# Optimization experiments

Measured on AMD Instinct MI355X. Metric: run time of the kernel, lower is better.

The kernel has to match this reference:

```python
import jax, jax.numpy as jnp
import numpy as np

B, L, HID, NH = 2, 2048, 1024, 16
HD = HID // NH  # 64


def setup_inputs() -> dict:
    key = jax.random.key(0)
    ks = jax.random.split(key, 12)
    s = 1.0 / np.sqrt(HID)
    query = jax.random.normal(ks[0], (B, L, HID), jnp.float32)
    key_t = jax.random.normal(ks[1], (B, L, HID), jnp.float32)
    value = jax.random.normal(ks[2], (B, L, HID), jnp.float32)
    # key padding mask: True = valid token; random lengths in [1024, 2048]
    lengths = jax.random.randint(ks[3], (B,), L // 2, L + 1)
    key_mask = jnp.arange(L)[None, :] < lengths[:, None]  # [B, K] bool
    # attn_mask: True = blocked (causal upper triangle), 2D branch [Q, K]
    attn_mask = jnp.triu(jnp.ones((L, L), jnp.bool_), k=1)
    Wq = jax.random.normal(ks[4], (HID, HID), jnp.float32) * s
    Wk = jax.random.normal(ks[5], (HID, HID), jnp.float32) * s
    Wv = jax.random.normal(ks[6], (HID, HID), jnp.float32) * s
    Wo = jax.random.normal(ks[7], (HID, HID), jnp.float32) * s
    bq = jax.random.normal(ks[8], (HID,), jnp.float32) * 0.01
    bk = jax.random.normal(ks[9], (HID,), jnp.float32) * 0.01
    bv = jax.random.normal(ks[10], (HID,), jnp.float32) * 0.01
    bo = jax.random.normal(ks[11], (HID,), jnp.float32) * 0.01
    return {"query": query, "key": key_t, "value": value,
            "key_mask": key_mask, "attn_mask": attn_mask,
            "Wq": Wq, "bq": bq, "Wk": Wk, "bk": bk,
            "Wv": Wv, "bv": bv, "Wo": Wo, "bo": bo}


def reference(query, key, value, key_mask, attn_mask,
              Wq, bq, Wk, bk, Wv, bv, Wo, bo):
    Bq, Q, _ = query.shape
    K = key.shape[1]
    # projections (torch Linear: x @ W.T + b), split heads -> [B, H, L, HD]
    def proj(x, W, b, L_):
        return (x @ W.T + b).reshape(Bq, L_, NH, HD).transpose(0, 2, 1, 3)
    q = proj(query, Wq, bq, Q)
    k = proj(key, Wk, bk, K)
    v = proj(value, Wv, bv, K)
    scores = jnp.einsum('bhqd,bhkd->bhqk', q, k) / np.sqrt(HD)
    blocked = attn_mask[None, None, :, :]                 # True = blocked
    kmask = key_mask[:, None, None, :]                    # True = valid
    valid = (~blocked) & kmask                            # [B,H,Q,K] (bcast)
    scores = jnp.where(blocked, -10000.0, scores)
    scores = jnp.where(kmask, scores, -10000.0)
    weights = jax.nn.softmax(scores, axis=-1)
    weights = weights * valid.astype(weights.dtype)
    weights = weights / jnp.maximum(weights.sum(-1, keepdims=True), 1e-6)
    attended = jnp.einsum('bhqk,bhkd->bhqd', weights, v)
    attended = attended.transpose(0, 2, 1, 3).reshape(Bq, Q, HID)
    return attended @ Wo.T + bo
```

## Files before the change

### kernel.cpp

```cpp
#include <hip/hip_runtime.h>
#include <hip/hip_bf16.h>
#include <stdint.h>


#define L_SEQ 2048
#define HID 1024
#define NHEAD 16
#define HD 64

typedef __attribute__((ext_vector_type(8))) short bf16x8;
typedef __attribute__((ext_vector_type(8))) unsigned short u16x8;
typedef __attribute__((ext_vector_type(4))) float f32x4;

__device__ __forceinline__ unsigned short f2bf(float f) {
  unsigned int u = __builtin_bit_cast(unsigned int, f);
  u += 0x7fffu + ((u >> 16) & 1u);
  return (unsigned short)(u >> 16);
}

__device__ __forceinline__ unsigned int pk2bf(float a, float b) {
  unsigned int r;
  asm("v_cvt_pk_bf16_f32 %0, %1, %2" : "=v"(r) : "v"(a), "v"(b));
  return r;
}

__device__ __forceinline__ void gl_lds16(const void* g, void* l) {
  __builtin_amdgcn_global_load_lds(
      (const __attribute__((address_space(1))) unsigned int*)(uintptr_t)g,
      (__attribute__((address_space(3))) unsigned int*)(uint32_t)(uintptr_t)l,
      16, 0, 0);
}

__device__ __forceinline__ f32x4 mfma16(bf16x8 a, bf16x8 b, f32x4 c) {
  return __builtin_amdgcn_mfma_f32_16x16x32_bf16(a, b, c, 0, 0, 0);
}

__global__ __launch_bounds__(256)
void convert_all_kernel(const float* __restrict__ q, const float* __restrict__ k,
                        const float* __restrict__ v, const float* __restrict__ wq,
                        const float* __restrict__ wk, const float* __restrict__ wv,
                        const float* __restrict__ wo, const unsigned int* __restrict__ km,
                        unsigned short* __restrict__ qb, unsigned short* __restrict__ kb,
                        unsigned short* __restrict__ vb, unsigned short* __restrict__ wqb,
                        unsigned short* __restrict__ wkb, unsigned short* __restrict__ wvb,
                        unsigned short* __restrict__ wob, int* __restrict__ lens) {
  __shared__ int red[256];
  const int bid = blockIdx.x;
  const int t = threadIdx.x;
  if (bid == 8192) {
    unsigned int w0 = km[0];
    bool u8mode = (w0 != 1u);
    for (int b = 0; b < 2; ++b) {
      int cnt = 0;
      if (u8mode) {
        const unsigned char* p = (const unsigned char*)km + b * L_SEQ;
        for (int i = t; i < L_SEQ; i += 256) cnt += (p[i] != 0) ? 1 : 0;
      } else {
        const unsigned int* p = km + b * L_SEQ;
        for (int i = t; i < L_SEQ; i += 256) cnt += (p[i] != 0) ? 1 : 0;
      }
      red[t] = cnt;
      __syncthreads();
      for (int s = 128; s > 0; s >>= 1) {
        if (t < s) red[t] += red[t + s];
        __syncthreads();
      }
      if (t == 0) lens[b] = red[0];
      __syncthreads();
    }
    return;
  }
  const float* src;
  unsigned short* dst;
  int base;
  if (bid < 6144) {
    int s = bid >> 11;
    base = (bid & 2047) * 2048;
    src = s == 0 ? q : (s == 1 ? k : v);
    dst = s == 0 ? qb : (s == 1 ? kb : vb);
  } else {
    int r = bid - 6144;
    int s = r >> 9;
    base = (r & 511) * 2048;
    src = s == 0 ? wq : (s == 1 ? wk : (s == 2 ? wv : wo));
    dst = s == 0 ? wqb : (s == 1 ? wkb : (s == 2 ? wvb : wob));
  }
  int i = base + t * 8;
  float4 a = *(const float4*)(src + i);
  float4 b4 = *(const float4*)(src + i + 4);
  u16x8 o;
  o[0] = f2bf(a.x); o[1] = f2bf(a.y); o[2] = f2bf(a.z); o[3] = f2bf(a.w);
  o[4] = f2bf(b4.x); o[5] = f2bf(b4.y); o[6] = f2bf(b4.z); o[7] = f2bf(b4.w);
  *(u16x8*)(dst + i) = o;
}

__device__ __forceinline__ void gemm128_bf_core(const unsigned short* __restrict__ A,
                                                const unsigned short* __restrict__ W,
                                                int m0, int n0, int K,
                                                unsigned short* As, unsigned short* Bs,
                                                f32x4 acc[4][4]) {
  const int tid = threadIdx.x;
  const int w = tid >> 6, lane = tid & 63;
  const int l15 = lane & 15, l4 = lane >> 4;
  const int wr = w >> 1, wc = w & 1;
#pragma unroll
  for (int i = 0; i < 4; ++i)
#pragma unroll
    for (int j = 0; j < 4; ++j) acc[i][j] = (f32x4){0.f, 0.f, 0.f, 0.f};

  const int nk = K >> 5;
#pragma unroll
  for (int i = 0; i < 2; ++i) {
    int c = i * 256 + tid;
    int row = c >> 2, col = (c & 3) * 8;
    gl_lds16(A + (size_t)(m0 + row) * K + col, (char*)As + (i * 256 + w * 64) * 16);
    gl_lds16(W + (size_t)(n0 + row) * K + col, (char*)Bs + (i * 256 + w * 64) * 16);
  }
  __syncthreads();

  int cur = 0;
  for (int t = 0; t < nk; ++t) {
    const int k0 = t * 32;
    if (t + 1 < nk) {
#pragma unroll
      for (int i = 0; i < 2; ++i) {
        int c = i * 256 + tid;
        int row = c >> 2, col = (c & 3) * 8;
        gl_lds16(A + (size_t)(m0 + row) * K + k0 + 32 + col,
                 (char*)As + (cur ^ 1) * 8192 + (i * 256 + w * 64) * 16);
        gl_lds16(W + (size_t)(n0 + row) * K + k0 + 32 + col,
                 (char*)Bs + (cur ^ 1) * 8192 + (i * 256 + w * 64) * 16);
      }
    }
    const unsigned short* Asb = As + cur * 4096;
    const unsigned short* Bsb = Bs + cur * 4096;
    bf16x8 af[4], bfr[4];
#pragma unroll
    for (int i = 0; i < 4; ++i)
      af[i] = *(const bf16x8*)(Asb + (wr * 64 + i * 16 + l15) * 32 + l4 * 8);
#pragma unroll
    for (int j = 0; j < 4; ++j)
      bfr[j] = *(const bf16x8*)(Bsb + (wc * 64 + j * 16 + l15) * 32 + l4 * 8);
    __builtin_amdgcn_s_setprio(1);
#pragma unroll
    for (int i = 0; i < 4; ++i)
#pragma unroll
      for (int j = 0; j < 4; ++j) acc[i][j] = mfma16(af[i], bfr[j], acc[i][j]);
    __builtin_amdgcn_s_setprio(0);
    __syncthreads();
    cur ^= 1;
  }
}

__global__ __launch_bounds__(256)
void qkv_gemm_kernel(const unsigned short* __restrict__ qb, const unsigned short* __restrict__ kb,
                     const unsigned short* __restrict__ vb, const unsigned short* __restrict__ wq,
                     const unsigned short* __restrict__ wk, const unsigned short* __restrict__ wv,
                     const float* __restrict__ bq, const float* __restrict__ bk,
                     const float* __restrict__ bv, unsigned short* __restrict__ Qp,
                     unsigned short* __restrict__ Kp, unsigned short* __restrict__ Vtp) {
  __shared__ unsigned short As[2 * 128 * 32];
  __shared__ unsigned short Bs[2 * 128 * 32];
  const int z = blockIdx.z;
  const unsigned short* A = z == 0 ? qb : (z == 1 ? kb : vb);
  const unsigned short* W = z == 0 ? wq : (z == 1 ? wk : wv);
  const float* bias = z == 0 ? bq : (z == 1 ? bk : bv);
  const int m0 = blockIdx.y * 128, n0 = blockIdx.x * 128;
  f32x4 acc[4][4];
  gemm128_bf_core(A, W, m0, n0, HID, As, Bs, acc);

  const int tid = threadIdx.x;
  const int w = tid >> 6, lane = tid & 63;
  const int l15 = lane & 15, l4 = lane >> 4;
  const int wr = w >> 1, wc = w & 1;
  const float scale = (z == 0) ? 0.125f * 1.44269504089f : 1.0f;
  if (z == 2) {
#pragma unroll
    for (int i = 0; i < 4; ++i)
#pragma unroll
      for (int j = 0; j < 4; ++j) {
        int grow0 = m0 + wr * 64 + i * 16 + l4 * 4;
        int gcol = n0 + wc * 64 + j * 16 + l15;
        float bv_ = bias[gcol];
        int bb = grow0 >> 11, ll0 = grow0 & 2047;
        int hh = gcol >> 6, d = gcol & 63;
        uint2 pw;
        pw.x = pk2bf(acc[i][j][0] + bv_, acc[i][j][1] + bv_);
        pw.y = pk2bf(acc[i][j][2] + bv_, acc[i][j][3] + bv_);
        *(uint2*)(&Vtp[((size_t)(bb * NHEAD + hh) * HD + d) * L_SEQ + ll0]) = pw;
      }
  } else {
    unsigned short* P = (z == 0) ? Qp : Kp;
#pragma unroll
    for (int i = 0; i < 4; ++i)
#pragma unroll
      for (int j = 0; j < 4; ++j)
#pragma unroll
        for (int r = 0; r < 4; ++r) {
          int grow = m0 + wr * 64 + i * 16 + l4 * 4 + r;
          int gcol = n0 + wc * 64 + j * 16 + l15;
          float v = (acc[i][j][r] + bias[gcol]) * scale;
          int bb = grow >> 11, ll = grow & 2047;
          int hh = gcol >> 6, d = gcol & 63;
          P[((size_t)(bb * NHEAD + hh) * L_SEQ + ll) * HD + d] = f2bf(v);
        }
  }
}

__global__ __launch_bounds__(256)
void out_gemm_kernel(const unsigned short* __restrict__ att, const unsigned short* __restrict__ wo,
                     const float* __restrict__ bo, float* __restrict__ out) {
  __shared__ unsigned short As[2 * 128 * 32];
  __shared__ unsigned short Bs[2 * 128 * 32];
  const int m0 = blockIdx.y * 128, n0 = blockIdx.x * 128;
  f32x4 acc[4][4];
  gemm128_bf_core(att, wo, m0, n0, HID, As, Bs, acc);

  const int tid = threadIdx.x;
  const int w = tid >> 6, lane = tid & 63;
  const int l15 = lane & 15, l4 = lane >> 4;
  const int wr = w >> 1, wc = w & 1;
#pragma unroll
  for (int i = 0; i < 4; ++i)
#pragma unroll
    for (int j = 0; j < 4; ++j)
#pragma unroll
      for (int r = 0; r < 4; ++r) {
        int grow = m0 + wr * 64 + i * 16 + l4 * 4 + r;
        int gcol = n0 + wc * 64 + j * 16 + l15;
        out[(size_t)grow * HID + gcol] = acc[i][j][r] + bo[gcol];
      }
}

__global__ __launch_bounds__(512)
void attn_kernel(const unsigned short* __restrict__ Qp, const unsigned short* __restrict__ Kp,
                 const unsigned short* __restrict__ Vtp, unsigned short* __restrict__ att,
                 const int* __restrict__ lens) {
  __shared__ unsigned short Ks[2][64 * 64];
  __shared__ unsigned short Vs[2][64 * 64];
  __shared__ unsigned short Ps[8][16 * 72];

  const int x = blockIdx.x, bh = blockIdx.y;
  const int b = bh >> 4, h = bh & 15;
  const int tid = threadIdx.x, w = tid >> 6, lane = tid & 63;
  const int l15 = lane & 15, l4 = lane >> 4;
  const int len = lens[b];
  const int sub = (w < 4) ? x : (31 - x);
  const int qw0 = sub * 64 + (w & 3) * 16;

  const unsigned short* Qg = Qp + (size_t)bh * L_SEQ * HD;
  const unsigned short* Kg = Kp + (size_t)bh * L_SEQ * HD;
  const unsigned short* Vg = Vtp + (size_t)bh * HD * L_SEQ;

  const int rr = tid >> 3, cb = tid & 7;
  const int swz = (cb ^ (rr & 7)) * 8;
  const unsigned short* KgRow = Kg + (size_t)rr * HD + swz;
  const unsigned short* VgRow = Vg + (size_t)rr * L_SEQ + swz;

  bf16x8 qf[2];
#pragma unroll
  for (int kk = 0; kk < 2; ++kk)
    qf[kk] = *(const bf16x8*)(Qg + (size_t)(qw0 + l15) * HD + kk * 32 + l4 * 8);

  f32x4 acc[4];
#pragma unroll
  for (int n = 0; n < 4; ++n) acc[n] = (f32x4){0.f, 0.f, 0.f, 0.f};
  float mq = -1e30f, lq = 0.f;

  int koff[4][2];
#pragma unroll
  for (int n = 0; n < 4; ++n)
#pragma unroll
    for (int kk = 0; kk < 2; ++kk) {
      int row = n * 16 + l15;
      koff[n][kk] = row * 128 + (((l4 + kk * 4) ^ (row & 7)) * 16);
    }

  const int len_r = ((len + 63) >> 6) << 6;
  const int hi_end = 64 * (32 - x);
  const int kv_end = (hi_end < len_r) ? hi_end : len_r;
  const int nt = kv_end >> 6;

  gl_lds16(KgRow, (char*)&Ks[0][0] + w * 1024);
  gl_lds16(VgRow, (char*)&Vs[0][0] + w * 1024);
  __syncthreads();

  int cur = 0;
  for (int t = 0; t < nt; ++t) {
    const int k0 = t * 64;
    if (t + 1 < nt) {
      const int k1 = k0 + 64;
      gl_lds16(KgRow + (size_t)k1 * HD, (char*)&Ks[cur ^ 1][0] + w * 1024);
      gl_lds16(VgRow + k1, (char*)&Vs[cur ^ 1][0] + w * 1024);
    }
    if (k0 <= qw0 + 15) {
      const char* Kb = (const char*)&Ks[cur][0];
      const char* Vb = (const char*)&Vs[cur][0];
      f32x4 s[4];
#pragma unroll
      for (int n = 0; n < 4; ++n) s[n] = (f32x4){0.f, 0.f, 0.f, 0.f};
      __builtin_amdgcn_s_setprio(1);
#pragma unroll
      for (int kk = 0; kk < 2; ++kk) {
#pragma unroll
        for (int n = 0; n < 4; ++n)
          s[n] = mfma16(*(const bf16x8*)(Kb + koff[n][kk]), qf[kk], s[n]);
      }
      __builtin_amdgcn_s_setprio(0);
      if (!(k0 + 63 <= qw0 && k0 + 64 <= len)) {
        const int qa = qw0 + l15;
#pragma unroll
        for (int n = 0; n < 4; ++n)
#pragma unroll
          for (int r = 0; r < 4; ++r) {
            int ka = k0 + n * 16 + l4 * 4 + r;
            if (ka > qa || ka >= len) s[n][r] = -1e30f;
          }
      }
      float v01 = fmaxf(fmaxf(s[0][0], s[0][1]), fmaxf(s[0][2], s[0][3]));
      float v23 = fmaxf(fmaxf(s[1][0], s[1][1]), fmaxf(s[1][2], s[1][3]));
      float v45 = fmaxf(fmaxf(s[2][0], s[2][1]), fmaxf(s[2][2], s[2][3]));
      float v67 = fmaxf(fmaxf(s[3][0], s[3][1]), fmaxf(s[3][2], s[3][3]));
      float v = fmaxf(fmaxf(v01, v23), fmaxf(v45, v67));
      v = fmaxf(v, __shfl_xor(v, 16));
      v = fmaxf(v, __shfl_xor(v, 32));
      if (!__all(v - mq <= 8.0f)) {
        float mnew = fmaxf(mq, v);
        float alpha = __builtin_amdgcn_exp2f(mq - mnew);
        mq = mnew;
        float ar[4];
#pragma unroll
        for (int r = 0; r < 4; ++r) ar[r] = __shfl(alpha, l4 * 4 + r, 64);
#pragma unroll
        for (int n = 0; n < 4; ++n)
#pragma unroll
          for (int r = 0; r < 4; ++r) acc[n][r] *= ar[r];
        lq *= alpha;
      }
      float rs = 0.f;
#pragma unroll
      for (int n = 0; n < 4; ++n)
#pragma unroll
        for (int r = 0; r < 4; ++r) {
          float p = __builtin_amdgcn_exp2f(s[n][r] - mq);
          s[n][r] = p;
          rs += p;
        }
      rs += __shfl_xor(rs, 16);
      rs += __shfl_xor(rs, 32);
      lq += rs;
#pragma unroll
      for (int n = 0; n < 4; ++n) {
        uint2 pw;
        pw.x = pk2bf(s[n][0], s[n][1]);
        pw.y = pk2bf(s[n][2], s[n][3]);
        *(uint2*)(&Ps[w][l15 * 72 + n * 16 + l4 * 4]) = pw;
      }
      bf16x8 pf[2];
#pragma unroll
      for (int kk = 0; kk < 2; ++kk)
        pf[kk] = *(const bf16x8*)(&Ps[w][l15 * 72 + kk * 32 + l4 * 8]);
      __builtin_amdgcn_s_setprio(1);
#pragma unroll
      for (int kk = 0; kk < 2; ++kk) {
#pragma unroll
        for (int n = 0; n < 4; ++n)
          acc[n] = mfma16(pf[kk], *(const bf16x8*)(Vb + koff[n][kk]), acc[n]);
      }
      __builtin_amdgcn_s_setprio(0);
    }
    __syncthreads();
    cur ^= 1;
  }

  float invq = 1.0f / lq;
  float invr[4];
#pragma unroll
  for (int r = 0; r < 4; ++r) invr[r] = __shfl(invq, l4 * 4 + r, 64);
#pragma unroll
  for (int r = 0; r < 4; ++r) {
    int qa = qw0 + l4 * 4 + r;
#pragma unroll
    for (int n = 0; n < 4; ++n)
      att[((size_t)(b * L_SEQ + qa)) * HID + h * HD + n * 16 + l15] = f2bf(acc[n][r] * invr[r]);
  }
}

extern "C" void kernel_launch(void* const* d_in, const int* in_sizes, int n_in,
                              void* d_out, int out_size, void* d_ws, size_t ws_size,
                              hipStream_t stream) {
  const float* query = (const float*)d_in[0];
  const float* key = (const float*)d_in[1];
  const float* value = (const float*)d_in[2];
  const unsigned int* key_mask = (const unsigned int*)d_in[3];
  const float* Wq = (const float*)d_in[5];
  const float* bq = (const float*)d_in[6];
  const float* Wk = (const float*)d_in[7];
  const float* bk = (const float*)d_in[8];
  const float* Wv = (const float*)d_in[9];
  const float* bv = (const float*)d_in[10];
  const float* Wo = (const float*)d_in[11];
  const float* bo = (const float*)d_in[12];

  char* ws = (char*)d_ws;
  const size_t SZ_X = (size_t)4096 * 1024 * 2;
  const size_t SZ_W = (size_t)1024 * 1024 * 2;
  unsigned short* qb = (unsigned short*)(ws);
  unsigned short* kb = (unsigned short*)(ws + SZ_X);
  unsigned short* vb = (unsigned short*)(ws + 2 * SZ_X);
  unsigned short* wqb = (unsigned short*)(ws + 3 * SZ_X);
  unsigned short* wkb = (unsigned short*)(ws + 3 * SZ_X + SZ_W);
  unsigned short* wvb = (unsigned short*)(ws + 3 * SZ_X + 2 * SZ_W);
  unsigned short* wob = (unsigned short*)(ws + 3 * SZ_X + 3 * SZ_W);
  unsigned short* Qp = (unsigned short*)(ws + 3 * SZ_X + 4 * SZ_W);
  unsigned short* Kp = (unsigned short*)(ws + 4 * SZ_X + 4 * SZ_W);
  unsigned short* Vtp = (unsigned short*)(ws + 5 * SZ_X + 4 * SZ_W);
  unsigned short* att = (unsigned short*)(ws + 6 * SZ_X + 4 * SZ_W);
  int* lens = (int*)(ws + 7 * SZ_X + 4 * SZ_W);

  convert_all_kernel<<<8193, 256, 0, stream>>>(query, key, value, Wq, Wk, Wv, Wo, key_mask,
                                               qb, kb, vb, wqb, wkb, wvb, wob, lens);
  qkv_gemm_kernel<<<dim3(8, 32, 3), 256, 0, stream>>>(qb, kb, vb, wqb, wkb, wvb, bq, bk, bv,
                                                      Qp, Kp, Vtp);
  attn_kernel<<<dim3(16, 32), 512, 0, stream>>>(Qp, Kp, Vtp, att, lens);
  out_gemm_kernel<<<dim3(8, 32), 256, 0, stream>>>(att, wob, bo, (float*)d_out);
}
```

Baseline: 129.7 us.

## Remap GEMM and attention blocks with XCD-aware swizzle, split attention into 256-thread blocks

```diff
diff --git a/kernel.cpp b/kernel.cpp
--- a/kernel.cpp
+++ b/kernel.cpp
@@ -161,11 +161,15 @@
                      unsigned short* __restrict__ Kp, unsigned short* __restrict__ Vtp) {
   __shared__ unsigned short As[2 * 128 * 32];
   __shared__ unsigned short Bs[2 * 128 * 32];
-  const int z = blockIdx.z;
+  const int id = blockIdx.x;
+  const int swz = (id & 7) * 96 + (id >> 3);
+  const int z = swz >> 8;
+  const int rem = swz & 255;
+  const int m0 = (rem >> 3) * 128, n0 = (rem & 7) * 128;
+
   const unsigned short* A = z == 0 ? qb : (z == 1 ? kb : vb);
   const unsigned short* W = z == 0 ? wq : (z == 1 ? wk : wv);
   const float* bias = z == 0 ? bq : (z == 1 ? bk : bv);
-  const int m0 = blockIdx.y * 128, n0 = blockIdx.x * 128;
   f32x4 acc[4][4];
   gemm128_bf_core(A, W, m0, n0, HID, As, Bs, acc);
 
@@ -212,7 +216,9 @@
                      const float* __restrict__ bo, float* __restrict__ out) {
   __shared__ unsigned short As[2 * 128 * 32];
   __shared__ unsigned short Bs[2 * 128 * 32];
-  const int m0 = blockIdx.y * 128, n0 = blockIdx.x * 128;
+  const int id = blockIdx.x;
+  const int swz = (id & 7) * 32 + (id >> 3);
+  const int m0 = (swz >> 3) * 128, n0 = (swz & 7) * 128;
   f32x4 acc[4][4];
   gemm128_bf_core(att, wo, m0, n0, HID, As, Bs, acc);
 
@@ -232,30 +238,35 @@
       }
 }
 
-__global__ __launch_bounds__(512)
+__global__ __launch_bounds__(256)
 void attn_kernel(const unsigned short* __restrict__ Qp, const unsigned short* __restrict__ Kp,
                  const unsigned short* __restrict__ Vtp, unsigned short* __restrict__ att,
                  const int* __restrict__ lens) {
   __shared__ unsigned short Ks[2][64 * 64];
   __shared__ unsigned short Vs[2][64 * 64];
-  __shared__ unsigned short Ps[8][16 * 72];
-
-  const int x = blockIdx.x, bh = blockIdx.y;
+  __shared__ unsigned short Ps[4][16 * 72];
+
+  const int id = blockIdx.x;
+  const int swz = (id & 7) * 128 + (id >> 3);
+  const int bh = swz >> 5;
+  const int sub = 31 - (swz & 31);
   const int b = bh >> 4, h = bh & 15;
   const int tid = threadIdx.x, w = tid >> 6, lane = tid & 63;
   const int l15 = lane & 15, l4 = lane >> 4;
   const int len = lens[b];
-  const int sub = (w < 4) ? x : (31 - x);
-  const int qw0 = sub * 64 + (w & 3) * 16;
+  const int qw0 = sub * 64 + w * 16;
 
   const unsigned short* Qg = Qp + (size_t)bh * L_SEQ * HD;
   const unsigned short* Kg = Kp + (size_t)bh * L_SEQ * HD;
   const unsigned short* Vg = Vtp + (size_t)bh * HD * L_SEQ;
 
-  const int rr = tid >> 3, cb = tid & 7;
-  const int swz = (cb ^ (rr & 7)) * 8;
-  const unsigned short* KgRow = Kg + (size_t)rr * HD + swz;
-  const unsigned short* VgRow = Vg + (size_t)rr * L_SEQ + swz;
+  const int c0 = tid, c1 = tid + 256;
+  const int rr0 = c0 >> 3, sz0 = ((c0 & 7) ^ (rr0 & 7)) * 8;
+  const int rr1 = c1 >> 3, sz1 = ((c1 & 7) ^ (rr1 & 7)) * 8;
+  const unsigned short* Kg0 = Kg + (size_t)rr0 * HD + sz0;
+  const unsigned short* Kg1 = Kg + (size_t)rr1 * HD + sz1;
+  const unsigned short* Vg0 = Vg + (size_t)rr0 * L_SEQ + sz0;
+  const unsigned short* Vg1 = Vg + (size_t)rr1 * L_SEQ + sz1;
 
   bf16x8 qf[2];
 #pragma unroll
@@ -277,23 +288,28 @@
     }
 
   const int len_r = ((len + 63) >> 6) << 6;
-  const int hi_end = 64 * (32 - x);
+  const int hi_end = (sub + 1) * 64;
   const int kv_end = (hi_end < len_r) ? hi_end : len_r;
   const int nt = kv_end >> 6;
 
-  gl_lds16(KgRow, (char*)&Ks[0][0] + w * 1024);
-  gl_lds16(VgRow, (char*)&Vs[0][0] + w * 1024);
+  gl_lds16(Kg0, (char*)&Ks[0][0] + c0 * 16);
+  gl_lds16(Kg1, (char*)&Ks[0][0] + c1 * 16);
+  gl_lds16(Vg0, (char*)&Vs[0][0] + c0 * 16);
+  gl_lds16(Vg1, (char*)&Vs[0][0] + c1 * 16);
   __syncthreads();
 
   int cur = 0;
   for (int t = 0; t < nt; ++t) {
     const int k0 = t * 64;
     if (t + 1 < nt) {
+      const size_t k1d = (size_t)(k0 + 64) * HD;
       const int k1 = k0 + 64;
-      gl_lds16(KgRow + (size_t)k1 * HD, (char*)&Ks[cur ^ 1][0] + w * 1024);
-      gl_lds16(VgRow + k1, (char*)&Vs[cur ^ 1][0] + w * 1024);
+      gl_lds16(Kg0 + k1d, (char*)&Ks[cur ^ 1][0] + c0 * 16);
+      gl_lds16(Kg1 + k1d, (char*)&Ks[cur ^ 1][0] + c1 * 16);
+      gl_lds16(Vg0 + k1, (char*)&Vs[cur ^ 1][0] + c0 * 16);
+      gl_lds16(Vg1 + k1, (char*)&Vs[cur ^ 1][0] + c1 * 16);
     }
-    if (k0 <= qw0 + 15) {
+    {
       const char* Kb = (const char*)&Ks[cur][0];
       const char* Vb = (const char*)&Vs[cur][0];
       f32x4 s[4];
@@ -420,8 +436,8 @@
 
   convert_all_kernel<<<8193, 256, 0, stream>>>(query, key, value, Wq, Wk, Wv, Wo, key_mask,
                                                qb, kb, vb, wqb, wkb, wvb, wob, lens);
-  qkv_gemm_kernel<<<dim3(8, 32, 3), 256, 0, stream>>>(qb, kb, vb, wqb, wkb, wvb, bq, bk, bv,
-                                                      Qp, Kp, Vtp);
-  attn_kernel<<<dim3(16, 32), 512, 0, stream>>>(Qp, Kp, Vtp, att, lens);
-  out_gemm_kernel<<<dim3(8, 32), 256, 0, stream>>>(att, wob, bo, (float*)d_out);
-}
+  qkv_gemm_kernel<<<768, 256, 0, stream>>>(qb, kb, vb, wqb, wkb, wvb, bq, bk, bv,
+                                           Qp, Kp, Vtp);
+  attn_kernel<<<1024, 256, 0, stream>>>(Qp, Kp, Vtp, att, lens);
+  out_gemm_kernel<<<256, 256, 0, stream>>>(att, wob, bo, (float*)d_out);
+}
```

Result: slower. 136.7 us (+5.3%).
